# Kernel tuning notes

Measured on AMD Instinct MI355X. Metric: run time of the kernel, lower is better.

The kernel has to match this reference:

```python
import jax, jax.numpy as jnp
import numpy as np
from jax import lax

V, E, H, T, B = 32000, 512, 512, 64, 64

def _xavier(key, shape):
    fan_out, fan_in = shape
    std = np.sqrt(2.0 / (fan_in + fan_out))
    return jax.random.normal(key, shape, dtype=jnp.float32) * std

def setup_inputs() -> dict:
    key = jax.random.key(0)
    ks = jax.random.split(key, 12)
    scale = np.sqrt(3.0 / E)
    emb = jax.random.uniform(ks[0], (V, E), minval=-scale, maxval=scale, dtype=jnp.float32)
    return {
        "emb": emb,                                   # frozen embedding table [V,E]
        "W_ih": _xavier(ks[1], (3 * H, E)),           # GRU input weights (r,z,n stacked)
        "W_hh": _xavier(ks[2], (3 * H, H)),           # GRU hidden weights
        "b_ih": jnp.zeros((3 * H,), jnp.float32),
        "b_hh": jnp.zeros((3 * H,), jnp.float32),
        "zt_W": _xavier(ks[3], (H, E + H)), "zt_b": jnp.zeros((H,), jnp.float32),
        "rt_W": _xavier(ks[4], (E, E + H)), "rt_b": jnp.zeros((E,), jnp.float32),
        "ht_W": _xavier(ks[5], (H, E + H)), "ht_b": jnp.zeros((H,), jnp.float32),
        "dec_W": _xavier(ks[6], (V, H)), "dec_b": jnp.zeros((V,), jnp.float32),
        "init_hidden": jnp.zeros((1, B, H), jnp.float32),
        "word": jax.random.randint(ks[7], (B,), 0, V),
        "seq": jax.random.randint(ks[8], (T, B), 0, V),
    }

def reference(emb, W_ih, W_hh, b_ih, b_hh, zt_W, zt_b, rt_W, rt_b, ht_W, ht_b,
              dec_W, dec_b, init_hidden, word, seq):
    word_emb = emb[word]          # [B,E] (frozen)
    seq_emb = emb[seq]            # [T,B,E]
    h0 = init_hidden[0]           # [B,H], single layer

    def step(h, x):
        # standard torch GRU cell
        gi = x @ W_ih.T + b_ih    # [B,3H]
        gh = h @ W_hh.T + b_hh
        i_r, i_z, i_n = jnp.split(gi, 3, axis=-1)
        h_r, h_z, h_n = jnp.split(gh, 3, axis=-1)
        r = jax.nn.sigmoid(i_r + h_r)
        z = jax.nn.sigmoid(i_z + h_z)
        n = jnp.tanh(i_n + r * h_n)
        h_gru = (1.0 - z) * n + z * h      # rnn output at this step
        # extra GRU-style gating with word embedding (use_g branch)
        inp_h = jnp.concatenate([word_emb, h_gru], axis=-1)      # [B,E+H]
        zt = jax.nn.sigmoid(inp_h @ zt_W.T + zt_b)               # [B,H]
        rt = jax.nn.sigmoid(inp_h @ rt_W.T + rt_b)               # [B,E]
        hcat = jnp.concatenate([rt * word_emb, h_gru], axis=-1)  # [B,E+H]
        h_tilde = jnp.tanh(hcat @ ht_W.T + ht_b)                 # [B,H]
        h_new = (1.0 - zt) * h_gru + zt * h_tilde
        return h_new, h_gru

    h_final, outs = lax.scan(step, h0, seq_emb)   # outs [T,B,H]
    flat = outs.reshape(-1, H)                    # [T*B,H]
    decoded = flat @ dec_W.T + dec_b              # [T*B,V]
    return decoded, h_final[None]                 # hidden [1,B,H]
```

## Files before the change

### kernel.cpp

```cpp
#include <hip/hip_runtime.h>
#include <stdint.h>

#define GAS __attribute__((address_space(1)))
#define LAS __attribute__((address_space(3)))

typedef __bf16 bf16x8 __attribute__((ext_vector_type(8)));
typedef _Float16 f16x8 __attribute__((ext_vector_type(8)));
typedef float f32x4 __attribute__((ext_vector_type(4)));

__device__ __forceinline__ unsigned short f2bf(float f) {
  unsigned u = __float_as_uint(f);
  unsigned r = (u + 0x7FFFu + ((u >> 16) & 1u)) >> 16;
  return (unsigned short)r;
}

__device__ __forceinline__ float sigmoidf(float x) {
  return 1.f / (1.f + expf(-x));
}

__device__ __forceinline__ void st2c(_Float16* p, _Float16 v) {
  unsigned short u = __builtin_bit_cast(unsigned short, v);
  __hip_atomic_store((unsigned short*)p, u, __ATOMIC_RELAXED, __HIP_MEMORY_SCOPE_AGENT);
}

__device__ __forceinline__ f16x8 ld16c(const _Float16* p) {
  f32x4 r;
  asm volatile("global_load_dwordx4 %0, %1, off sc0 sc1"
               : "=v"(r) : "v"(p) : "memory");
  return __builtin_bit_cast(f16x8, r);
}

__global__ __launch_bounds__(128) void k_gather(
    const float* __restrict__ emb, const int* __restrict__ seq,
    const int* __restrict__ word, unsigned short* __restrict__ xbf,
    float* __restrict__ wemb) {
  int row = blockIdx.x;
  int tid = threadIdx.x;
  if (row < 4096) {
    const float* src = emb + (size_t)seq[row] * 512;
    unsigned short* dst = xbf + (size_t)row * 512;
    for (int e = tid; e < 512; e += 128) dst[e] = f2bf(src[e]);
  } else {
    int b = row - 4096;
    const float* src = emb + (size_t)word[b] * 512;
    float* dst = wemb + (size_t)b * 512;
    for (int e = tid; e < 512; e += 128) dst[e] = src[e];
  }
}

__global__ __launch_bounds__(128) void k_conv(
    const float* __restrict__ Wih, const float* __restrict__ decW,
    unsigned short* __restrict__ wih_bf, unsigned short* __restrict__ dec_bf) {
  int row = blockIdx.x;
  int tid = threadIdx.x;
  if (row < 1536) {
    const float* s = Wih + (size_t)row * 512;
    unsigned short* d = wih_bf + (size_t)row * 512;
    for (int e = tid; e < 512; e += 128) d[e] = f2bf(s[e]);
  } else {
    int o = row - 1536;
    const float* s = decW + (size_t)o * 512;
    unsigned short* d = dec_bf + (size_t)o * 512;
    for (int e = tid; e < 512; e += 128) d[e] = f2bf(s[e]);
  }
}

__global__ __launch_bounds__(256) void k_pre(
    const float* __restrict__ ztW, const float* __restrict__ ztb,
    const float* __restrict__ rtW, const float* __restrict__ rtb,
    const float* __restrict__ wemb, float* __restrict__ ztp,
    float* __restrict__ rtp) {
  int idx = blockIdx.x * 256 + threadIdx.x;
  int b = idx >> 10, o = idx & 1023;
  const float4* we = (const float4*)(wemb + (size_t)b * 512);
  const float4* wr;
  float acc;
  if (o < 512) { wr = (const float4*)(ztW + (size_t)o * 1024); acc = ztb[o]; }
  else { wr = (const float4*)(rtW + (size_t)(o - 512) * 1024); acc = rtb[o - 512]; }
  for (int c = 0; c < 128; ++c) {
    float4 w = wr[c], e = we[c];
    acc += w.x * e.x + w.y * e.y + w.z * e.z + w.w * e.w;
  }
  if (o < 512) ztp[(size_t)b * 512 + o] = acc;
  else rtp[(size_t)b * 512 + (o - 512)] = acc;
}

__global__ __launch_bounds__(256) void k_gemm_bt(
    const unsigned short* __restrict__ A, const unsigned short* __restrict__ B,
    float* __restrict__ C, const float* __restrict__ bias,
    int M, int N, int K) {
  __shared__ __align__(16) unsigned short As[128 * 32];
  __shared__ __align__(16) unsigned short Bs[128 * 32];
  int nt = N >> 7;
  int nwg = gridDim.x;
  int bid = blockIdx.x;
  int swz = (bid & 7) * (nwg >> 3) + (bid >> 3);
  int m0 = (swz / nt) << 7, n0 = (swz % nt) << 7;
  int tid = threadIdx.x;
  int l = tid & 63, w = tid >> 6;
  int wr = w >> 1, wc = w & 1;
  int lr = l & 15, lk = l >> 4;
  f32x4 acc[4][4] = {};
  for (int k0 = 0; k0 < K; k0 += 32) {
#pragma unroll
    for (int i = 0; i < 2; ++i) {
      int c = w * 2 + i;
      int off = c * 1024 + l * 16;
      int row = off >> 6, kb = off & 63;
      const char* ga = (const char*)A + ((size_t)(m0 + row) * K + k0) * 2 + kb;
      const char* gb = (const char*)B + ((size_t)(n0 + row) * K + k0) * 2 + kb;
      __builtin_amdgcn_global_load_lds((const GAS void*)ga,
                                       (LAS void*)((char*)As + c * 1024), 16, 0, 0);
      __builtin_amdgcn_global_load_lds((const GAS void*)gb,
                                       (LAS void*)((char*)Bs + c * 1024), 16, 0, 0);
    }
    asm volatile("s_waitcnt vmcnt(0)" ::: "memory");
    __syncthreads();
    bf16x8 af[4], bfr[4];
#pragma unroll
    for (int i = 0; i < 4; ++i)
      af[i] = *(const bf16x8*)&As[(wr * 64 + i * 16 + lr) * 32 + lk * 8];
#pragma unroll
    for (int i = 0; i < 4; ++i)
      bfr[i] = *(const bf16x8*)&Bs[(wc * 64 + i * 16 + lr) * 32 + lk * 8];
#pragma unroll
    for (int i = 0; i < 4; ++i)
#pragma unroll
      for (int jj = 0; jj < 4; ++jj)
        acc[i][jj] = __builtin_amdgcn_mfma_f32_16x16x32_bf16(af[i], bfr[jj], acc[i][jj], 0, 0, 0);
    __syncthreads();
  }
#pragma unroll
  for (int jj = 0; jj < 4; ++jj) {
    int col = n0 + wc * 64 + jj * 16 + lr;
    float bv = bias ? bias[col] : 0.f;
#pragma unroll
    for (int i = 0; i < 4; ++i) {
      int rb = m0 + wr * 64 + i * 16 + lk * 4;
#pragma unroll
      for (int q = 0; q < 4; ++q)
        C[(size_t)(rb + q) * N + col] = acc[i][jj][q] + bv;
    }
  }
}

struct RnnP {
  const float *Whh, *ztW, *rtW, *htW;
  const float *gi, *ztp, *rtp, *wemb, *inith, *bhh, *htb;
  _Float16 *hcur, *hgru, *rw;
  unsigned short *outsb;
  float *hfin;
  unsigned *flags;
};

__device__ __forceinline__ void gbarf(unsigned* flags, int g, unsigned phase) {
  asm volatile("s_waitcnt vmcnt(0)" ::: "memory");
  __syncthreads();
  if (threadIdx.x == 0)
    __hip_atomic_store(flags + (size_t)g * 16, phase, __ATOMIC_RELAXED,
                       __HIP_MEMORY_SCOPE_AGENT);
  int lane = threadIdx.x & 63;
  unsigned v;
  do {
    v = (lane < 32)
            ? __hip_atomic_load(flags + (size_t)lane * 16, __ATOMIC_RELAXED,
                                __HIP_MEMORY_SCOPE_AGENT)
            : phase;
  } while (!__all(v >= phase));
}

template <int NT>
__device__ __forceinline__ void mm_phase(f32x4* acc, const _Float16* A,
                                         const _Float16* WLrow, int w, int lr, int lk) {
  f16x8 af[16];
  const _Float16* arow = A + ((size_t)(16 * w + lr)) * 512 + lk * 8;
#pragma unroll
  for (int c = 0; c < 16; ++c) af[c] = ld16c(arow + c * 32);
  asm volatile("s_waitcnt vmcnt(0)" ::: "memory");
  __builtin_amdgcn_sched_barrier(0);
#pragma unroll
  for (int c = 0; c < 16; ++c) {
#pragma unroll
    for (int n = 0; n < NT; ++n) {
      f16x8 bb = *(const f16x8*)(WLrow + (n * 16 + lr) * 520 + c * 32 + lk * 8);
      acc[n] = __builtin_amdgcn_mfma_f32_16x16x32_f16(af[c], bb, acc[n], 0, 0, 0);
    }
  }
}

__global__ __launch_bounds__(256) void k_rnn2(RnnP p) {
  const int g = blockIdx.x, tid = threadIdx.x;
  const int w = tid >> 6, l = tid & 63;
  const int lr = l & 15, lk = l >> 4;
  __shared__ _Float16 WL[112 * 520];
  for (int idx = tid; idx < 112 * 512; idx += 256) {
    int rr = idx >> 9, e = idx & 511;
    const float* src;
    if (rr < 48) {
      int gate = rr >> 4, i = rr & 15;
      src = p.Whh + ((size_t)(gate * 512 + g * 16 + i)) * 512 + e;
    } else if (rr < 96) {
      int r2 = rr - 48, gate = r2 >> 4, i = r2 & 15;
      const float* base = gate == 0 ? p.ztW : (gate == 1 ? p.rtW : p.htW);
      src = base + ((size_t)(g * 16 + i)) * 1024 + 512 + e;
    } else {
      int i = rr - 96;
      src = p.htW + ((size_t)(g * 16 + i)) * 1024 + e;
    }
    WL[rr * 520 + e] = (_Float16)(*src);
  }
  const int j = g * 16 + lr;
  const int brow = 16 * w + lk * 4;
  f32x4 hprev, zp, rp, wev;
#pragma unroll
  for (int q = 0; q < 4; ++q) {
    int b = brow + q;
    hprev[q] = p.inith[(size_t)b * 512 + j];
    zp[q] = p.ztp[(size_t)b * 512 + j];
    rp[q] = p.rtp[(size_t)b * 512 + j];
    wev[q] = p.wemb[(size_t)b * 512 + j];
    st2c(&p.hcur[(size_t)b * 512 + j], (_Float16)hprev[q]);
  }
  const float br = p.bhh[j], bz = p.bhh[512 + j], bn = p.bhh[1024 + j];
  const float bht = p.htb[j];
  float gir[12];
#pragma unroll
  for (int q = 0; q < 4; ++q) {
    const float* git = p.gi + (size_t)(brow + q) * 1536;
    gir[q * 3 + 0] = git[j];
    gir[q * 3 + 1] = git[512 + j];
    gir[q * 3 + 2] = git[1024 + j];
  }
  unsigned ph = 1;
  gbarf(p.flags, g, ph); ph++;
  for (int t = 0; t < 64; ++t) {
    f32x4 acc1[3] = {};
    mm_phase<3>(acc1, p.hcur, &WL[0], w, lr, lk);
    f32x4 hg;
#pragma unroll
    for (int q = 0; q < 4; ++q) {
      int b = brow + q;
      float r = sigmoidf(gir[q * 3 + 0] + br + acc1[0][q]);
      float z = sigmoidf(gir[q * 3 + 1] + bz + acc1[1][q]);
      float n = tanhf(gir[q * 3 + 2] + r * (acc1[2][q] + bn));
      float hgq = (1.f - z) * n + z * hprev[q];
      hg[q] = hgq;
      st2c(&p.hgru[(size_t)b * 512 + j], (_Float16)hgq);
      p.outsb[((size_t)t * 64 + b) * 512 + j] = f2bf(hgq);
    }
    gbarf(p.flags, g, ph); ph++;
    f32x4 acc2[3] = {};
    mm_phase<3>(acc2, p.hgru, &WL[48 * 520], w, lr, lk);
    f32x4 zt, htB;
#pragma unroll
    for (int q = 0; q < 4; ++q) {
      int b = brow + q;
      float ztq = sigmoidf(zp[q] + acc2[0][q]);
      float rtq = sigmoidf(rp[q] + acc2[1][q]);
      zt[q] = ztq;
      htB[q] = acc2[2][q];
      st2c(&p.rw[(size_t)b * 512 + j], (_Float16)(rtq * wev[q]));
    }
    gbarf(p.flags, g, ph); ph++;
    if (t < 63) {
      const float* git = p.gi + (size_t)(t + 1) * 64 * 1536;
#pragma unroll
      for (int q = 0; q < 4; ++q) {
        const float* gb = git + (size_t)(brow + q) * 1536;
        gir[q * 3 + 0] = gb[j];
        gir[q * 3 + 1] = gb[512 + j];
        gir[q * 3 + 2] = gb[1024 + j];
      }
    }
    f32x4 acc3[1] = {};
    mm_phase<1>(acc3, p.rw, &WL[96 * 520], w, lr, lk);
#pragma unroll
    for (int q = 0; q < 4; ++q) {
      int b = brow + q;
      float htl = tanhf(acc3[0][q] + htB[q] + bht);
      float hn2 = (1.f - zt[q]) * hg[q] + zt[q] * htl;
      hprev[q] = hn2;
      if (t < 63) st2c(&p.hcur[(size_t)b * 512 + j], (_Float16)hn2);
      else p.hfin[(size_t)b * 512 + j] = hn2;
    }
    if (t < 63) { gbarf(p.flags, g, ph); ph++; }
  }
}

extern "C" void kernel_launch(void* const* d_in, const int* in_sizes, int n_in,
                              void* d_out, int out_size, void* d_ws, size_t ws_size,
                              hipStream_t stream) {
  const float* emb   = (const float*)d_in[0];
  const float* Wih   = (const float*)d_in[1];
  const float* Whh   = (const float*)d_in[2];
  const float* bih   = (const float*)d_in[3];
  const float* bhh   = (const float*)d_in[4];
  const float* ztW   = (const float*)d_in[5];
  const float* ztb   = (const float*)d_in[6];
  const float* rtW   = (const float*)d_in[7];
  const float* rtb   = (const float*)d_in[8];
  const float* htW   = (const float*)d_in[9];
  const float* htb   = (const float*)d_in[10];
  const float* decW  = (const float*)d_in[11];
  const float* decb  = (const float*)d_in[12];
  const float* inith = (const float*)d_in[13];
  const int* word    = (const int*)d_in[14];
  const int* seq     = (const int*)d_in[15];
  float* out = (float*)d_out;

  char* ws = (char*)d_ws;
  size_t off = 0;
  auto alloc = [&](size_t bytes) {
    size_t o = off;
    off += (bytes + 255) & ~(size_t)255;
    return o;
  };
  unsigned short* xbf   = (unsigned short*)(ws + alloc(4096ull * 512 * 2));
  unsigned short* wihbf = (unsigned short*)(ws + alloc(1536ull * 512 * 2));
  unsigned short* decbf = (unsigned short*)(ws + alloc(32000ull * 512 * 2));
  float* wemb           = (float*)(ws + alloc(64ull * 512 * 4));
  float* ztp            = (float*)(ws + alloc(64ull * 512 * 4));
  float* rtp            = (float*)(ws + alloc(64ull * 512 * 4));
  float* gi             = (float*)(ws + alloc(4096ull * 1536 * 4));
  unsigned short* outsb = (unsigned short*)(ws + alloc(4096ull * 512 * 2));
  _Float16* hcur        = (_Float16*)(ws + alloc(64ull * 512 * 2));
  _Float16* hgru        = (_Float16*)(ws + alloc(64ull * 512 * 2));
  _Float16* rw          = (_Float16*)(ws + alloc(64ull * 512 * 2));
  unsigned* flags       = (unsigned*)(ws + alloc(32 * 64));

  hipLaunchKernelGGL(k_gather, dim3(4160), dim3(128), 0, stream,
                     emb, seq, word, xbf, wemb);
  hipLaunchKernelGGL(k_conv, dim3(33536), dim3(128), 0, stream,
                     Wih, decW, wihbf, decbf);
  hipLaunchKernelGGL(k_pre, dim3(256), dim3(256), 0, stream,
                     ztW, ztb, rtW, rtb, wemb, ztp, rtp);
  hipLaunchKernelGGL(k_gemm_bt, dim3(384), dim3(256), 0, stream,
                     xbf, wihbf, gi, bih, 4096, 1536, 512);
  hipMemsetAsync(flags, 0, 32 * 64, stream);
  RnnP p{Whh, ztW, rtW, htW, gi, ztp, rtp, wemb, inith, bhh, htb,
         hcur, hgru, rw, outsb, out + 4096ull * 32000, flags};
  hipLaunchKernelGGL(k_rnn2, dim3(32), dim3(256), 0, stream, p);
  hipLaunchKernelGGL(k_gemm_bt, dim3(8000), dim3(256), 0, stream,
                     outsb, decbf, out, decb, 4096, 32000, 512);
}
```

Baseline: 1.326 ms.

## Fuse recurrence and decoder GEMM into one persistent kernel with per-wave flags

Merges the 32-block GRU recurrence and the large decoder GEMM into one 256-block kernel. The 224 extra blocks poll per-timestep flags and compute each timestep's 64x32000 logits as soon as that step's GRU output is written, overlapping the decoder with the serial recurrence. The global barrier is also replaced with per-wave flag signalling, where each wave polls only the band of flags it depends on, and A-loads use immediate offsets. Risks include the decoder blocks competing for bandwidth with the latency-bound recurrence, and a deadlock if all 256 blocks are not co-resident.

New measurement: 1.429 ms. 7.8% more time.

```diff
diff --git a/kernel.cpp b/kernel.cpp
--- a/kernel.cpp
+++ b/kernel.cpp
@@ -7,6 +7,7 @@
 typedef __bf16 bf16x8 __attribute__((ext_vector_type(8)));
 typedef _Float16 f16x8 __attribute__((ext_vector_type(8)));
 typedef float f32x4 __attribute__((ext_vector_type(4)));
+typedef unsigned u32x4 __attribute__((ext_vector_type(4)));
 
 __device__ __forceinline__ unsigned short f2bf(float f) {
   unsigned u = __float_as_uint(f);
@@ -22,11 +23,26 @@
   unsigned short u = __builtin_bit_cast(unsigned short, v);
   __hip_atomic_store((unsigned short*)p, u, __ATOMIC_RELAXED, __HIP_MEMORY_SCOPE_AGENT);
 }
-
-__device__ __forceinline__ f16x8 ld16c(const _Float16* p) {
-  f32x4 r;
+__device__ __forceinline__ void stu2c(unsigned short* p, unsigned short v) {
+  __hip_atomic_store(p, v, __ATOMIC_RELAXED, __HIP_MEMORY_SCOPE_AGENT);
+}
+__device__ __forceinline__ void stf_mall(unsigned* p, unsigned v) {
+  __hip_atomic_store(p, v, __ATOMIC_RELAXED, __HIP_MEMORY_SCOPE_AGENT);
+}
+__device__ __forceinline__ unsigned ldf_mall(const unsigned* p) {
+  return __hip_atomic_load(p, __ATOMIC_RELAXED, __HIP_MEMORY_SCOPE_AGENT);
+}
+__device__ __forceinline__ u32x4 ld16_mall(const void* p) {
+  u32x4 r;
   asm volatile("global_load_dwordx4 %0, %1, off sc0 sc1"
                : "=v"(r) : "v"(p) : "memory");
+  return r;
+}
+template <int OFF>
+__device__ __forceinline__ f16x8 ldh8_mall(const _Float16* p) {
+  u32x4 r;
+  asm volatile("global_load_dwordx4 %0, %1, off offset:%2 sc0 sc1"
+               : "=v"(r) : "v"(p), "n"(OFF) : "memory");
   return __builtin_bit_cast(f16x8, r);
 }
 
@@ -144,38 +160,36 @@
   }
 }
 
-struct RnnP {
+struct MegaP {
   const float *Whh, *ztW, *rtW, *htW;
   const float *gi, *ztp, *rtp, *wemb, *inith, *bhh, *htb;
-  _Float16 *hcur, *hgru, *rw;
+  _Float16 *hcurF, *hgruF, *rwF;
   unsigned short *outsb;
   float *hfin;
   unsigned *flags;
+  const unsigned short *decbf;
+  const float *decb;
+  float *outC;
 };
 
-__device__ __forceinline__ void gbarf(unsigned* flags, int g, unsigned phase) {
-  asm volatile("s_waitcnt vmcnt(0)" ::: "memory");
-  __syncthreads();
-  if (threadIdx.x == 0)
-    __hip_atomic_store(flags + (size_t)g * 16, phase, __ATOMIC_RELAXED,
-                       __HIP_MEMORY_SCOPE_AGENT);
-  int lane = threadIdx.x & 63;
-  unsigned v;
-  do {
-    v = (lane < 32)
-            ? __hip_atomic_load(flags + (size_t)lane * 16, __ATOMIC_RELAXED,
-                                __HIP_MEMORY_SCOPE_AGENT)
-            : phase;
-  } while (!__all(v >= phase));
+__device__ __forceinline__ void poll_band(const unsigned* flags, int w, int l,
+                                          unsigned tgt) {
+  const unsigned* fp = flags + ((size_t)((l & 31) * 4 + w)) * 16;
+  for (;;) {
+    unsigned v = ldf_mall(fp);
+    if (__all((int)(v >= tgt))) break;
+  }
 }
 
 template <int NT>
-__device__ __forceinline__ void mm_phase(f32x4* acc, const _Float16* A,
-                                         const _Float16* WLrow, int w, int lr, int lk) {
+__device__ __forceinline__ void mm_mall(f32x4* acc, const _Float16* A,
+                                        const _Float16* WLrow, int w, int lr, int lk) {
   f16x8 af[16];
   const _Float16* arow = A + ((size_t)(16 * w + lr)) * 512 + lk * 8;
-#pragma unroll
-  for (int c = 0; c < 16; ++c) af[c] = ld16c(arow + c * 32);
+#define LDA(c) af[c] = ldh8_mall<(c) * 64>(arow);
+  LDA(0) LDA(1) LDA(2) LDA(3) LDA(4) LDA(5) LDA(6) LDA(7)
+  LDA(8) LDA(9) LDA(10) LDA(11) LDA(12) LDA(13) LDA(14) LDA(15)
+#undef LDA
   asm volatile("s_waitcnt vmcnt(0)" ::: "memory");
   __builtin_amdgcn_sched_barrier(0);
 #pragma unroll
@@ -188,102 +202,201 @@
   }
 }
 
-__global__ __launch_bounds__(256) void k_rnn2(RnnP p) {
-  const int g = blockIdx.x, tid = threadIdx.x;
+__global__ __launch_bounds__(256) void k_mega(MegaP p) {
+  __shared__ __align__(16) char LSD[116480];
+  const int tid = threadIdx.x;
   const int w = tid >> 6, l = tid & 63;
   const int lr = l & 15, lk = l >> 4;
-  __shared__ _Float16 WL[112 * 520];
-  for (int idx = tid; idx < 112 * 512; idx += 256) {
-    int rr = idx >> 9, e = idx & 511;
-    const float* src;
-    if (rr < 48) {
-      int gate = rr >> 4, i = rr & 15;
-      src = p.Whh + ((size_t)(gate * 512 + g * 16 + i)) * 512 + e;
-    } else if (rr < 96) {
-      int r2 = rr - 48, gate = r2 >> 4, i = r2 & 15;
-      const float* base = gate == 0 ? p.ztW : (gate == 1 ? p.rtW : p.htW);
-      src = base + ((size_t)(g * 16 + i)) * 1024 + 512 + e;
-    } else {
-      int i = rr - 96;
-      src = p.htW + ((size_t)(g * 16 + i)) * 1024 + e;
-    }
-    WL[rr * 520 + e] = (_Float16)(*src);
-  }
-  const int j = g * 16 + lr;
-  const int brow = 16 * w + lk * 4;
-  f32x4 hprev, zp, rp, wev;
-#pragma unroll
-  for (int q = 0; q < 4; ++q) {
-    int b = brow + q;
-    hprev[q] = p.inith[(size_t)b * 512 + j];
-    zp[q] = p.ztp[(size_t)b * 512 + j];
-    rp[q] = p.rtp[(size_t)b * 512 + j];
-    wev[q] = p.wemb[(size_t)b * 512 + j];
-    st2c(&p.hcur[(size_t)b * 512 + j], (_Float16)hprev[q]);
-  }
-  const float br = p.bhh[j], bz = p.bhh[512 + j], bn = p.bhh[1024 + j];
-  const float bht = p.htb[j];
-  float gir[12];
-#pragma unroll
-  for (int q = 0; q < 4; ++q) {
-    const float* git = p.gi + (size_t)(brow + q) * 1536;
-    gir[q * 3 + 0] = git[j];
-    gir[q * 3 + 1] = git[512 + j];
-    gir[q * 3 + 2] = git[1024 + j];
-  }
-  unsigned ph = 1;
-  gbarf(p.flags, g, ph); ph++;
-  for (int t = 0; t < 64; ++t) {
-    f32x4 acc1[3] = {};
-    mm_phase<3>(acc1, p.hcur, &WL[0], w, lr, lk);
-    f32x4 hg;
+
+  if (blockIdx.x < 32) {
+    const int g = blockIdx.x;
+    _Float16* WL = (_Float16*)LSD;
+    for (int idx = tid; idx < 112 * 512; idx += 256) {
+      int rr = idx >> 9, e = idx & 511;
+      const float* src;
+      if (rr < 48) {
+        int gate = rr >> 4, i = rr & 15;
+        src = p.Whh + ((size_t)(gate * 512 + g * 16 + i)) * 512 + e;
+      } else if (rr < 96) {
+        int r2 = rr - 48, gate = r2 >> 4, i = r2 & 15;
+        const float* base = gate == 0 ? p.ztW : (gate == 1 ? p.rtW : p.htW);
+        src = base + ((size_t)(g * 16 + i)) * 1024 + 512 + e;
+      } else {
+        int i = rr - 96;
+        src = p.htW + ((size_t)(g * 16 + i)) * 1024 + e;
+      }
+      WL[rr * 520 + e] = (_Float16)(*src);
+    }
+    const int j = g * 16 + lr;
+    const int brow = 16 * w + lk * 4;
+    f32x4 hprev, zp, rp, wev;
 #pragma unroll
     for (int q = 0; q < 4; ++q) {
       int b = brow + q;
-      float r = sigmoidf(gir[q * 3 + 0] + br + acc1[0][q]);
-      float z = sigmoidf(gir[q * 3 + 1] + bz + acc1[1][q]);
-      float n = tanhf(gir[q * 3 + 2] + r * (acc1[2][q] + bn));
-      float hgq = (1.f - z) * n + z * hprev[q];
-      hg[q] = hgq;
-      st2c(&p.hgru[(size_t)b * 512 + j], (_Float16)hgq);
-      p.outsb[((size_t)t * 64 + b) * 512 + j] = f2bf(hgq);
-    }
-    gbarf(p.flags, g, ph); ph++;
-    f32x4 acc2[3] = {};
-    mm_phase<3>(acc2, p.hgru, &WL[48 * 520], w, lr, lk);
-    f32x4 zt, htB;
+      hprev[q] = p.inith[(size_t)b * 512 + j];
+      zp[q] = p.ztp[(size_t)b * 512 + j];
+      rp[q] = p.rtp[(size_t)b * 512 + j];
+      wev[q] = p.wemb[(size_t)b * 512 + j];
+      st2c(&p.hcurF[(size_t)b * 512 + j], (_Float16)hprev[q]);
+    }
+    const float br = p.bhh[j], bz = p.bhh[512 + j], bn = p.bhh[1024 + j];
+    const float bht = p.htb[j];
+    float gir[12];
 #pragma unroll
     for (int q = 0; q < 4; ++q) {
-      int b = brow + q;
-      float ztq = sigmoidf(zp[q] + acc2[0][q]);
-      float rtq = sigmoidf(rp[q] + acc2[1][q]);
-      zt[q] = ztq;
-      htB[q] = acc2[2][q];
-      st2c(&p.rw[(size_t)b * 512 + j], (_Float16)(rtq * wev[q]));
-    }
-    gbarf(p.flags, g, ph); ph++;
-    if (t < 63) {
-      const float* git = p.gi + (size_t)(t + 1) * 64 * 1536;
+      const float* git = p.gi + (size_t)(brow + q) * 1536;
+      gir[q * 3 + 0] = git[j];
+      gir[q * 3 + 1] = git[512 + j];
+      gir[q * 3 + 2] = git[1024 + j];
+    }
+    __syncthreads();
+    asm volatile("s_waitcnt vmcnt(0)" ::: "memory");
+    if (tid == 0) stf_mall(p.flags + (size_t)(g * 4 + 0) * 16, 1u);
+    else if (tid == 64) stf_mall(p.flags + (size_t)(g * 4 + 1) * 16, 1u);
+    else if (tid == 128) stf_mall(p.flags + (size_t)(g * 4 + 2) * 16, 1u);
+    else if (tid == 192) stf_mall(p.flags + (size_t)(g * 4 + 3) * 16, 1u);
+
+    for (int t = 0; t < 64; ++t) {
+      const unsigned base = 3u * (unsigned)t;
+      poll_band(p.flags, w, l, base + 1);
+      f32x4 acc1[3] = {};
+      mm_mall<3>(acc1, p.hcurF, &WL[0], w, lr, lk);
+      f32x4 hg;
 #pragma unroll
       for (int q = 0; q < 4; ++q) {
-        const float* gb = git + (size_t)(brow + q) * 1536;
-        gir[q * 3 + 0] = gb[j];
-        gir[q * 3 + 1] = gb[512 + j];
-        gir[q * 3 + 2] = gb[1024 + j];
-      }
-    }
-    f32x4 acc3[1] = {};
-    mm_phase<1>(acc3, p.rw, &WL[96 * 520], w, lr, lk);
-#pragma unroll
-    for (int q = 0; q < 4; ++q) {
-      int b = brow + q;
-      float htl = tanhf(acc3[0][q] + htB[q] + bht);
-      float hn2 = (1.f - zt[q]) * hg[q] + zt[q] * htl;
-      hprev[q] = hn2;
-      if (t < 63) st2c(&p.hcur[(size_t)b * 512 + j], (_Float16)hn2);
-      else p.hfin[(size_t)b * 512 + j] = hn2;
-    }
-    if (t < 63) { gbarf(p.flags, g, ph); ph++; }
+        int b = brow + q;
+        float r = sigmoidf(gir[q * 3 + 0] + br + acc1[0][q]);
+        float z = sigmoidf(gir[q * 3 + 1] + bz + acc1[1][q]);
+        float n = tanhf(gir[q * 3 + 2] + r * (acc1[2][q] + bn));
+        float hgq = (1.f - z) * n + z * hprev[q];
+        hg[q] = hgq;
+        st2c(&p.hgruF[(size_t)b * 512 + j], (_Float16)hgq);
+        stu2c(&p.outsb[((size_t)t * 64 + b) * 512 + j], f2bf(hgq));
+      }
+      asm volatile("s_waitcnt vmcnt(0)" ::: "memory");
+      if (l == 0) stf_mall(p.flags + ((size_t)(g * 4 + w)) * 16, base + 2);
+      poll_band(p.flags, w, l, base + 2);
+      f32x4 acc2[3] = {};
+      mm_mall<3>(acc2, p.hgruF, &WL[48 * 520], w, lr, lk);
+      f32x4 zt, htB;
+#pragma unroll
+      for (int q = 0; q < 4; ++q) {
+        int b = brow + q;
+        float ztq = sigmoidf(zp[q] + acc2[0][q]);
+        float rtq = sigmoidf(rp[q] + acc2[1][q]);
+        zt[q] = ztq;
+        htB[q] = acc2[2][q];
+        st2c(&p.rwF[(size_t)b * 512 + j], (_Float16)(rtq * wev[q]));
+      }
+      asm volatile("s_waitcnt vmcnt(0)" ::: "memory");
+      if (l == 0) stf_mall(p.flags + ((size_t)(g * 4 + w)) * 16, base + 3);
+      if (t < 63) {
+        const float* git = p.gi + (size_t)(t + 1) * 64 * 1536;
+#pragma unroll
+        for (int q = 0; q < 4; ++q) {
+          const float* gb = git + (size_t)(brow + q) * 1536;
+          gir[q * 3 + 0] = gb[j];
+          gir[q * 3 + 1] = gb[512 + j];
+          gir[q * 3 + 2] = gb[1024 + j];
+        }
+      }
+      poll_band(p.flags, w, l, base + 3);
+      f32x4 acc3[1] = {};
+      mm_mall<1>(acc3, p.rwF, &WL[96 * 520], w, lr, lk);
+#pragma unroll
+      for (int q = 0; q < 4; ++q) {
+        int b = brow + q;
+        float htl = tanhf(acc3[0][q] + htB[q] + bht);
+        float hn2 = (1.f - zt[q]) * hg[q] + zt[q] * htl;
+        hprev[q] = hn2;
+        if (t < 63) st2c(&p.hcurF[(size_t)b * 512 + j], (_Float16)hn2);
+        else p.hfin[(size_t)b * 512 + j] = hn2;
+      }
+      if (t < 63) {
+        asm volatile("s_waitcnt vmcnt(0)" ::: "memory");
+        if (l == 0) stf_mall(p.flags + ((size_t)(g * 4 + w)) * 16, base + 4);
+      }
+    }
+  } else {
+    const int d = blockIdx.x - 32;
+    unsigned short* As = (unsigned short*)LSD;
+    unsigned short* Bs = (unsigned short*)(LSD + 64 * 520 * 2);
+    for (int t = 0; t < 64; ++t) {
+      const unsigned tgt = 3u * (unsigned)t + 2u;
+      {
+        const unsigned* f0 = p.flags + (size_t)l * 16;
+        const unsigned* f1 = p.flags + (size_t)(l + 64) * 16;
+        for (;;) {
+          unsigned a = ldf_mall(f0);
+          unsigned b = ldf_mall(f1);
+          if (__all((int)(a >= tgt && b >= tgt))) break;
+        }
+      }
+      __syncthreads();
+      {
+        u32x4 av[8];
+#pragma unroll
+        for (int it = 0; it < 8; ++it) {
+          int fi = (tid + 256 * it) * 8;
+          av[it] = ld16_mall(p.outsb + ((size_t)t * 64 + (fi >> 9)) * 512 + (fi & 511));
+        }
+        asm volatile("s_waitcnt vmcnt(0)" ::: "memory");
+#pragma unroll
+        for (int it = 0; it < 8; ++it) {
+          int fi = (tid + 256 * it) * 8;
+          *(u32x4*)&As[(fi >> 9) * 520 + (fi & 511)] = av[it];
+        }
+#pragma unroll
+        for (int it = 8; it < 16; ++it) {
+          int fi = (tid + 256 * it) * 8;
+          av[it - 8] = ld16_mall(p.outsb + ((size_t)t * 64 + (fi >> 9)) * 512 + (fi & 511));
+        }
+        asm volatile("s_waitcnt vmcnt(0)" ::: "memory");
+#pragma unroll
+        for (int it = 8; it < 16; ++it) {
+          int fi = (tid + 256 * it) * 8;
+          *(u32x4*)&As[(fi >> 9) * 520 + (fi & 511)] = av[it - 8];
+        }
+      }
+      __syncthreads();
+#pragma unroll 1
+      for (int tix = 0; tix < 2; ++tix) {
+        int tile = d + tix * 224;
+        if (tile >= 250) break;
+        int n0 = tile * 128;
+        f32x4 acc[8] = {};
+        for (int k0 = 0; k0 < 512; k0 += 32) {
+#pragma unroll
+          for (int i = 0; i < 2; ++i) {
+            int c = w * 2 + i;
+            int off = c * 1024 + l * 16;
+            int row = off >> 6, kb = off & 63;
+            const char* gb = (const char*)p.decbf + ((size_t)(n0 + row) * 512 + k0) * 2 + kb;
+            __builtin_amdgcn_global_load_lds((const GAS void*)gb,
+                                             (LAS void*)((char*)Bs + c * 1024), 16, 0, 0);
+          }
+          asm volatile("s_waitcnt vmcnt(0)" ::: "memory");
+          __syncthreads();
+          bf16x8 af = *(const bf16x8*)&As[(16 * w + lr) * 520 + k0 + lk * 8];
+#pragma unroll
+          for (int n = 0; n < 8; ++n) {
+            bf16x8 bfr = *(const bf16x8*)&Bs[(n * 16 + lr) * 32 + lk * 8];
+            acc[n] = __builtin_amdgcn_mfma_f32_16x16x32_bf16(af, bfr, acc[n], 0, 0, 0);
+          }
+          __syncthreads();
+        }
+#pragma unroll
+        for (int n = 0; n < 8; ++n) {
+          int col = n0 + n * 16 + lr;
+          float bv = p.decb[col];
+#pragma unroll
+          for (int q = 0; q < 4; ++q) {
+            int row = t * 64 + 16 * w + lk * 4 + q;
+            p.outC[(size_t)row * 32000 + col] = acc[n][q] + bv;
+          }
+        }
+      }
+    }
   }
 }
 
@@ -323,10 +436,10 @@
   float* rtp            = (float*)(ws + alloc(64ull * 512 * 4));
   float* gi             = (float*)(ws + alloc(4096ull * 1536 * 4));
   unsigned short* outsb = (unsigned short*)(ws + alloc(4096ull * 512 * 2));
-  _Float16* hcur        = (_Float16*)(ws + alloc(64ull * 512 * 2));
-  _Float16* hgru        = (_Float16*)(ws + alloc(64ull * 512 * 2));
-  _Float16* rw          = (_Float16*)(ws + alloc(64ull * 512 * 2));
-  unsigned* flags       = (unsigned*)(ws + alloc(32 * 64));
+  _Float16* hcurF       = (_Float16*)(ws + alloc(64ull * 512 * 2));
+  _Float16* hgruF       = (_Float16*)(ws + alloc(64ull * 512 * 2));
+  _Float16* rwF         = (_Float16*)(ws + alloc(64ull * 512 * 2));
+  unsigned* flags       = (unsigned*)(ws + alloc(128 * 64));
 
   hipLaunchKernelGGL(k_gather, dim3(4160), dim3(128), 0, stream,
                      emb, seq, word, xbf, wemb);
@@ -336,10 +449,9 @@
                      ztW, ztb, rtW, rtb, wemb, ztp, rtp);
   hipLaunchKernelGGL(k_gemm_bt, dim3(384), dim3(256), 0, stream,
                      xbf, wihbf, gi, bih, 4096, 1536, 512);
-  hipMemsetAsync(flags, 0, 32 * 64, stream);
-  RnnP p{Whh, ztW, rtW, htW, gi, ztp, rtp, wemb, inith, bhh, htb,
-         hcur, hgru, rw, outsb, out + 4096ull * 32000, flags};
-  hipLaunchKernelGGL(k_rnn2, dim3(32), dim3(256), 0, stream, p);
-  hipLaunchKernelGGL(k_gemm_bt, dim3(8000), dim3(256), 0, stream,
-                     outsb, decbf, out, decb, 4096, 32000, 512);
-}
+  hipMemsetAsync(flags, 0, 128 * 64, stream);
+  MegaP p{Whh, ztW, rtW, htW, gi, ztp, rtp, wemb, inith, bhh, htb,
+          hcurF, hgruF, rwF, outsb, out + 4096ull * 32000, flags,
+          decbf, decb, out};
+  hipLaunchKernelGGL(k_mega, dim3(256), dim3(256), 0, stream, p);
+}
```

## Replace block-wide grid barrier with per-wave band flags in persistent RNN kernel

Applied to the files above, without the earlier changes.

Swaps the block-level global barrier (syncthreads plus one flag per block) for per-wave flags. Each wave polls only the 32 flags for its own 16-row batch band, so waves advance independently instead of waiting for the whole grid. The outsb store and the next-step gi prefetch move to after the flag publish, so they overlap with the wait. Flag stores are now issued by each wave without a block sync, which relies on the vmcnt wait for ordering and adds some risk of a memory-ordering bug.

New measurement: 1.421 ms. +7.2%, slower.

```diff
diff --git a/kernel.cpp b/kernel.cpp
--- a/kernel.cpp
+++ b/kernel.cpp
@@ -7,6 +7,7 @@
 typedef __bf16 bf16x8 __attribute__((ext_vector_type(8)));
 typedef _Float16 f16x8 __attribute__((ext_vector_type(8)));
 typedef float f32x4 __attribute__((ext_vector_type(4)));
+typedef unsigned u32x4 __attribute__((ext_vector_type(4)));
 
 __device__ __forceinline__ unsigned short f2bf(float f) {
   unsigned u = __float_as_uint(f);
@@ -22,11 +23,17 @@
   unsigned short u = __builtin_bit_cast(unsigned short, v);
   __hip_atomic_store((unsigned short*)p, u, __ATOMIC_RELAXED, __HIP_MEMORY_SCOPE_AGENT);
 }
-
-__device__ __forceinline__ f16x8 ld16c(const _Float16* p) {
-  f32x4 r;
-  asm volatile("global_load_dwordx4 %0, %1, off sc0 sc1"
-               : "=v"(r) : "v"(p) : "memory");
+__device__ __forceinline__ void stf_mall(unsigned* p, unsigned v) {
+  __hip_atomic_store(p, v, __ATOMIC_RELAXED, __HIP_MEMORY_SCOPE_AGENT);
+}
+__device__ __forceinline__ unsigned ldf_mall(const unsigned* p) {
+  return __hip_atomic_load(p, __ATOMIC_RELAXED, __HIP_MEMORY_SCOPE_AGENT);
+}
+template <int OFF>
+__device__ __forceinline__ f16x8 ldh8_mall(const _Float16* p) {
+  u32x4 r;
+  asm volatile("global_load_dwordx4 %0, %1, off offset:%2 sc0 sc1"
+               : "=v"(r) : "v"(p), "n"(OFF) : "memory");
   return __builtin_bit_cast(f16x8, r);
 }
 
@@ -147,35 +154,30 @@
 struct RnnP {
   const float *Whh, *ztW, *rtW, *htW;
   const float *gi, *ztp, *rtp, *wemb, *inith, *bhh, *htb;
-  _Float16 *hcur, *hgru, *rw;
+  _Float16 *hcurF, *hgruF, *rwF;
   unsigned short *outsb;
   float *hfin;
   unsigned *flags;
 };
 
-__device__ __forceinline__ void gbarf(unsigned* flags, int g, unsigned phase) {
-  asm volatile("s_waitcnt vmcnt(0)" ::: "memory");
-  __syncthreads();
-  if (threadIdx.x == 0)
-    __hip_atomic_store(flags + (size_t)g * 16, phase, __ATOMIC_RELAXED,
-                       __HIP_MEMORY_SCOPE_AGENT);
-  int lane = threadIdx.x & 63;
-  unsigned v;
-  do {
-    v = (lane < 32)
-            ? __hip_atomic_load(flags + (size_t)lane * 16, __ATOMIC_RELAXED,
-                                __HIP_MEMORY_SCOPE_AGENT)
-            : phase;
-  } while (!__all(v >= phase));
+__device__ __forceinline__ void poll_band(const unsigned* flags, int w, int l,
+                                          unsigned tgt) {
+  const unsigned* fp = flags + w * 32 + (l & 31);
+  for (;;) {
+    unsigned v = ldf_mall(fp);
+    if (__all((int)(v >= tgt))) break;
+  }
 }
 
 template <int NT>
-__device__ __forceinline__ void mm_phase(f32x4* acc, const _Float16* A,
-                                         const _Float16* WLrow, int w, int lr, int lk) {
+__device__ __forceinline__ void mm_mall(f32x4* acc, const _Float16* A,
+                                        const _Float16* WLrow, int w, int lr, int lk) {
   f16x8 af[16];
   const _Float16* arow = A + ((size_t)(16 * w + lr)) * 512 + lk * 8;
-#pragma unroll
-  for (int c = 0; c < 16; ++c) af[c] = ld16c(arow + c * 32);
+#define LDA(c) af[c] = ldh8_mall<(c) * 64>(arow);
+  LDA(0) LDA(1) LDA(2) LDA(3) LDA(4) LDA(5) LDA(6) LDA(7)
+  LDA(8) LDA(9) LDA(10) LDA(11) LDA(12) LDA(13) LDA(14) LDA(15)
+#undef LDA
   asm volatile("s_waitcnt vmcnt(0)" ::: "memory");
   __builtin_amdgcn_sched_barrier(0);
 #pragma unroll
@@ -188,10 +190,11 @@
   }
 }
 
-__global__ __launch_bounds__(256) void k_rnn2(RnnP p) {
+__global__ __launch_bounds__(256) void k_rnn5(RnnP p) {
   const int g = blockIdx.x, tid = threadIdx.x;
   const int w = tid >> 6, l = tid & 63;
   const int lr = l & 15, lk = l >> 4;
+  unsigned* myflag = p.flags + w * 32 + g;
   __shared__ _Float16 WL[112 * 520];
   for (int idx = tid; idx < 112 * 512; idx += 256) {
     int rr = idx >> 9, e = idx & 511;
@@ -219,7 +222,7 @@
     zp[q] = p.ztp[(size_t)b * 512 + j];
     rp[q] = p.rtp[(size_t)b * 512 + j];
     wev[q] = p.wemb[(size_t)b * 512 + j];
-    st2c(&p.hcur[(size_t)b * 512 + j], (_Float16)hprev[q]);
+    st2c(&p.hcurF[(size_t)b * 512 + j], (_Float16)hprev[q]);
   }
   const float br = p.bhh[j], bz = p.bhh[512 + j], bn = p.bhh[1024 + j];
   const float bht = p.htb[j];
@@ -231,11 +234,14 @@
     gir[q * 3 + 1] = git[512 + j];
     gir[q * 3 + 2] = git[1024 + j];
   }
-  unsigned ph = 1;
-  gbarf(p.flags, g, ph); ph++;
+  __syncthreads();
+  if (l == 0) stf_mall(myflag, 1u);
+
   for (int t = 0; t < 64; ++t) {
+    const unsigned base = 3u * (unsigned)t;
+    poll_band(p.flags, w, l, base + 1);
     f32x4 acc1[3] = {};
-    mm_phase<3>(acc1, p.hcur, &WL[0], w, lr, lk);
+    mm_mall<3>(acc1, p.hcurF, &WL[0], w, lr, lk);
     f32x4 hg;
 #pragma unroll
     for (int q = 0; q < 4; ++q) {
@@ -245,12 +251,26 @@
       float n = tanhf(gir[q * 3 + 2] + r * (acc1[2][q] + bn));
       float hgq = (1.f - z) * n + z * hprev[q];
       hg[q] = hgq;
-      st2c(&p.hgru[(size_t)b * 512 + j], (_Float16)hgq);
-      p.outsb[((size_t)t * 64 + b) * 512 + j] = f2bf(hgq);
-    }
-    gbarf(p.flags, g, ph); ph++;
+      st2c(&p.hgruF[(size_t)b * 512 + j], (_Float16)hgq);
+    }
+    asm volatile("s_waitcnt vmcnt(0)" ::: "memory");
+    if (l == 0) stf_mall(myflag, base + 2);
+#pragma unroll
+    for (int q = 0; q < 4; ++q)
+      p.outsb[((size_t)t * 64 + brow + q) * 512 + j] = f2bf(hg[q]);
+    if (t < 63) {
+      const float* git = p.gi + (size_t)(t + 1) * 64 * 1536;
+#pragma unroll
+      for (int q = 0; q < 4; ++q) {
+        const float* gb = git + (size_t)(brow + q) * 1536;
+        gir[q * 3 + 0] = gb[j];
+        gir[q * 3 + 1] = gb[512 + j];
+        gir[q * 3 + 2] = gb[1024 + j];
+      }
+    }
+    poll_band(p.flags, w, l, base + 2);
     f32x4 acc2[3] = {};
-    mm_phase<3>(acc2, p.hgru, &WL[48 * 520], w, lr, lk);
+    mm_mall<3>(acc2, p.hgruF, &WL[48 * 520], w, lr, lk);
     f32x4 zt, htB;
 #pragma unroll
     for (int q = 0; q < 4; ++q) {
@@ -259,31 +279,26 @@
       float rtq = sigmoidf(rp[q] + acc2[1][q]);
       zt[q] = ztq;
       htB[q] = acc2[2][q];
-      st2c(&p.rw[(size_t)b * 512 + j], (_Float16)(rtq * wev[q]));
-    }
-    gbarf(p.flags, g, ph); ph++;
-    if (t < 63) {
-      const float* git = p.gi + (size_t)(t + 1) * 64 * 1536;
-#pragma unroll
-      for (int q = 0; q < 4; ++q) {
-        const float* gb = git + (size_t)(brow + q) * 1536;
-        gir[q * 3 + 0] = gb[j];
-        gir[q * 3 + 1] = gb[512 + j];
-        gir[q * 3 + 2] = gb[1024 + j];
-      }
-    }
+      st2c(&p.rwF[(size_t)b * 512 + j], (_Float16)(rtq * wev[q]));
+    }
+    asm volatile("s_waitcnt vmcnt(0)" ::: "memory");
+    if (l == 0) stf_mall(myflag, base + 3);
+    poll_band(p.flags, w, l, base + 3);
     f32x4 acc3[1] = {};
-    mm_phase<1>(acc3, p.rw, &WL[96 * 520], w, lr, lk);
+    mm_mall<1>(acc3, p.rwF, &WL[96 * 520], w, lr, lk);
 #pragma unroll
     for (int q = 0; q < 4; ++q) {
       int b = brow + q;
       float htl = tanhf(acc3[0][q] + htB[q] + bht);
       float hn2 = (1.f - zt[q]) * hg[q] + zt[q] * htl;
       hprev[q] = hn2;
-      if (t < 63) st2c(&p.hcur[(size_t)b * 512 + j], (_Float16)hn2);
+      if (t < 63) st2c(&p.hcurF[(size_t)b * 512 + j], (_Float16)hn2);
       else p.hfin[(size_t)b * 512 + j] = hn2;
     }
-    if (t < 63) { gbarf(p.flags, g, ph); ph++; }
+    if (t < 63) {
+      asm volatile("s_waitcnt vmcnt(0)" ::: "memory");
+      if (l == 0) stf_mall(myflag, base + 4);
+    }
   }
 }
 
@@ -323,10 +338,10 @@
   float* rtp            = (float*)(ws + alloc(64ull * 512 * 4));
   float* gi             = (float*)(ws + alloc(4096ull * 1536 * 4));
   unsigned short* outsb = (unsigned short*)(ws + alloc(4096ull * 512 * 2));
-  _Float16* hcur        = (_Float16*)(ws + alloc(64ull * 512 * 2));
-  _Float16* hgru        = (_Float16*)(ws + alloc(64ull * 512 * 2));
-  _Float16* rw          = (_Float16*)(ws + alloc(64ull * 512 * 2));
-  unsigned* flags       = (unsigned*)(ws + alloc(32 * 64));
+  _Float16* hcurF       = (_Float16*)(ws + alloc(64ull * 512 * 2));
+  _Float16* hgruF       = (_Float16*)(ws + alloc(64ull * 512 * 2));
+  _Float16* rwF         = (_Float16*)(ws + alloc(64ull * 512 * 2));
+  unsigned* flags       = (unsigned*)(ws + alloc(512));
 
   hipLaunchKernelGGL(k_gather, dim3(4160), dim3(128), 0, stream,
                      emb, seq, word, xbf, wemb);
@@ -336,10 +351,10 @@
                      ztW, ztb, rtW, rtb, wemb, ztp, rtp);
   hipLaunchKernelGGL(k_gemm_bt, dim3(384), dim3(256), 0, stream,
                      xbf, wihbf, gi, bih, 4096, 1536, 512);
-  hipMemsetAsync(flags, 0, 32 * 64, stream);
+  hipMemsetAsync(flags, 0, 512, stream);
   RnnP p{Whh, ztW, rtW, htW, gi, ztp, rtp, wemb, inith, bhh, htb,
-         hcur, hgru, rw, outsb, out + 4096ull * 32000, flags};
-  hipLaunchKernelGGL(k_rnn2, dim3(32), dim3(256), 0, stream, p);
+         hcurF, hgruF, rwF, outsb, out + 4096ull * 32000, flags};
+  hipLaunchKernelGGL(k_rnn5, dim3(32), dim3(256), 0, stream, p);
   hipLaunchKernelGGL(k_gemm_bt, dim3(8000), dim3(256), 0, stream,
                      outsb, decbf, out, decb, 4096, 32000, 512);
 }
```
